# Kernel optimization log

Hardware: AMD Instinct MI355X
Metric: run time of the kernel (lower is better)

## Reference

```python
import jax, jax.numpy as jnp
import numpy as np

HEADS = 24
KV_HEADS = 6
HEAD_DIM = 64


def _partial_rope(x, cos, sin):
    # x: [B, H, S, head_dim]; cos/sin: [S, rot_dim]; rotate first rot_dim dims
    rot_dim = cos.shape[-1]
    x_rot, x_pass = x[..., :rot_dim], x[..., rot_dim:]
    half = rot_dim // 2
    # use_real_unbind_dim=-2: reshape (..., 2, half) then unbind -> first/second half
    x_real, x_imag = x_rot[..., :half], x_rot[..., half:]
    x_rotated = jnp.concatenate([-x_imag, x_real], axis=-1)
    out = x_rot * cos[None, None] + x_rotated * sin[None, None]
    return jnp.concatenate([out, x_pass], axis=-1)


def setup_inputs() -> dict:
    key = jax.random.key(0)
    ks = jax.random.split(key, 8)
    B, S, D = 2, 2048, 1536
    kv_dim = KV_HEADS * HEAD_DIM
    rot_dim = 32
    hidden_states = jax.random.normal(ks[0], (B, S, D), dtype=jnp.float32)
    # realistic rotary cos/sin from inv-freq angles
    pos = jnp.arange(S, dtype=jnp.float32)
    inv_freq = 1.0 / (10000.0 ** (jnp.arange(0, rot_dim, 2, dtype=jnp.float32) / rot_dim))
    ang = pos[:, None] * inv_freq[None, :]  # [S, rot_dim//2]
    ang = jnp.concatenate([ang, ang], axis=-1)  # [S, rot_dim]
    cos, sin = jnp.cos(ang), jnp.sin(ang)
    Wq = jax.random.normal(ks[1], (D, D), dtype=jnp.float32) * 0.02
    Wk = jax.random.normal(ks[2], (D, kv_dim), dtype=jnp.float32) * 0.02
    Wv = jax.random.normal(ks[3], (D, kv_dim), dtype=jnp.float32) * 0.02
    Wo = jax.random.normal(ks[4], (D, D), dtype=jnp.float32) * 0.02
    bo = jnp.zeros((D,), dtype=jnp.float32)
    return {"hidden_states": hidden_states, "cos": cos, "sin": sin,
            "Wq": Wq, "Wk": Wk, "Wv": Wv, "Wo": Wo, "bo": bo}


def reference(hidden_states, cos, sin, Wq, Wk, Wv, Wo, bo):
    B, S, D = hidden_states.shape
    residual = hidden_states
    q = hidden_states @ Wq  # [B,S,D]
    k = hidden_states @ Wk  # [B,S,kv_dim]
    v = hidden_states @ Wv
    q = q.reshape(B, S, HEADS, HEAD_DIM).transpose(0, 2, 1, 3)       # [B,H,S,d]
    k = k.reshape(B, S, KV_HEADS, HEAD_DIM).transpose(0, 2, 1, 3)    # [B,Hkv,S,d]
    v = v.reshape(B, S, KV_HEADS, HEAD_DIM).transpose(0, 2, 1, 3)
    rep = HEADS // KV_HEADS
    k = jnp.repeat(k, rep, axis=1)  # GQA repeat_interleave -> [B,H,S,d]
    v = jnp.repeat(v, rep, axis=1)
    # partial RoPE on query and key (self-attention)
    q = _partial_rope(q, cos, sin)
    k = _partial_rope(k, cos, sin)
    scale = 1.0 / jnp.sqrt(jnp.float32(HEAD_DIM))
    scores = jnp.einsum('bhqd,bhkd->bhqk', q, k) * scale
    probs = jax.nn.softmax(scores, axis=-1)
    out = jnp.einsum('bhqk,bhkd->bhqd', probs, v)
    out = out.transpose(0, 2, 1, 3).reshape(B, S, D)
    out = out @ Wo + bo
    return out + residual
```

## Files before the change

### kernel.cpp

```cpp
#include <hip/hip_runtime.h>

#define HEADS 24
#define KVH   6
#define HD    64
#define BB    2
#define SS    2048
#define DD    1536
#define KVD   384
#define QKD   1920
#define MM    4096

typedef unsigned short ushort_t;
typedef __attribute__((ext_vector_type(8))) short short8;
typedef __attribute__((ext_vector_type(4))) float f32x4;

__device__ __forceinline__ ushort_t f2bf(float f) {
    union { float f; unsigned u; } v; v.f = f;
    return (ushort_t)((v.u + 0x8000u) >> 16);
}
__device__ __forceinline__ ushort_t f2bf_trunc(float f) {
    union { float f; unsigned u; } v; v.f = f;
    return (ushort_t)(v.u >> 16);
}
__device__ __forceinline__ unsigned pk2(float a, float b) {
    union { float f; unsigned u; } x, y; x.f = a; y.f = b;
    return ((x.u + 0x8000u) >> 16) | (((y.u + 0x8000u) >> 16) << 16);
}
#if __has_builtin(__builtin_amdgcn_exp2f)
#define EXP2(x) __builtin_amdgcn_exp2f(x)
#else
#define EXP2(x) exp2f(x)
#endif
__device__ __forceinline__ void glds16(const void* g, void* l) {
    __builtin_amdgcn_global_load_lds(
        (const __attribute__((address_space(1))) void*)g,
        (__attribute__((address_space(3))) void*)l, 16, 0, 0);
}

__device__ __forceinline__ void tconv_body(const float* __restrict__ in,
                                           ushort_t* __restrict__ out,
                                           int R, int C, int cb, int rb)
{
    __shared__ ushort_t tile[32][33];
    const int tx = threadIdx.x & 31, ty = threadIdx.x >> 5;
    const int c0 = cb * 32, r0 = rb * 32;
#pragma unroll
    for (int i = 0; i < 4; ++i)
        tile[ty + i * 8][tx] = f2bf(in[(size_t)(r0 + ty + i * 8) * C + c0 + tx]);
    __syncthreads();
#pragma unroll
    for (int i = 0; i < 4; ++i)
        out[(size_t)(c0 + ty + i * 8) * R + r0 + tx] = tile[tx][ty + i * 8];
}

#define NCVT (MM * DD / 4 / 256)
__global__ __launch_bounds__(256) void k_prep(const float* __restrict__ HS,
                                              const float* __restrict__ Wq,
                                              const float* __restrict__ Wk,
                                              const float* __restrict__ Wv,
                                              const float* __restrict__ Wo,
                                              ushort_t* __restrict__ Xbf,
                                              ushort_t* __restrict__ Wqt,
                                              ushort_t* __restrict__ Wkt,
                                              ushort_t* __restrict__ Wvt,
                                              ushort_t* __restrict__ Wot)
{
    int bid = blockIdx.x;
    if (bid < NCVT) {
        int i = bid * 256 + threadIdx.x;
        float4 v = ((const float4*)HS)[i];
        uint2 o = { pk2(v.x, v.y), pk2(v.z, v.w) };
        ((uint2*)Xbf)[i] = o;
        return;
    }
    bid -= NCVT;
    if (bid < 2304) { tconv_body(Wq, Wqt, DD, DD,  bid % 48, bid / 48); return; }
    bid -= 2304;
    if (bid < 576)  { tconv_body(Wk, Wkt, DD, KVD, bid % 12, bid / 12); return; }
    bid -= 576;
    if (bid < 576)  { tconv_body(Wv, Wvt, DD, KVD, bid % 12, bid / 12); return; }
    bid -= 576;
    tconv_body(Wo, Wot, DD, DD, bid % 48, bid / 48);
}

__global__ __launch_bounds__(256) void k_qkv_mfma(const ushort_t* __restrict__ Xbf,
                                                  const ushort_t* __restrict__ Wqt,
                                                  const ushort_t* __restrict__ Wkt,
                                                  const float* __restrict__ cosb,
                                                  const float* __restrict__ sinb,
                                                  ushort_t* __restrict__ QKVb)
{
    __shared__ ushort_t As[128][32];
    __shared__ ushort_t Bs[128][32];
    const int t = threadIdx.x, lane = t & 63, wave = t >> 6;
    const int n16 = lane & 15, quad = lane >> 4;
    const int wr = wave >> 1, wc = wave & 1;
    const int nt = blockIdx.x;
    const int n0 = nt * 128;
    const int m0 = blockIdx.y * 128;
    const ushort_t* Bt; int nl, isq;
    if (nt < 12) { Bt = Wqt; nl = n0;      isq = 1; }
    else         { Bt = Wkt; nl = n0 - DD; isq = 0; }

    const int srow = lane >> 2;
    const int scol = (lane & 3) * 8;
    const size_t aoff0 = (size_t)(m0 + wave * 16 + srow) * DD + scol;
    const size_t aoff1 = (size_t)(m0 + (wave + 4) * 16 + srow) * DD + scol;
    const size_t boff0 = (size_t)(nl + wave * 16 + srow) * DD + scol;
    const size_t boff1 = (size_t)(nl + (wave + 4) * 16 + srow) * DD + scol;
    ushort_t* lA0 = &As[wave * 16][0];
    ushort_t* lA1 = &As[(wave + 4) * 16][0];
    ushort_t* lB0 = &Bs[wave * 16][0];
    ushort_t* lB1 = &Bs[(wave + 4) * 16][0];

    f32x4 acc[4][4] = {};
    for (int k0 = 0; k0 < DD; k0 += 32) {
        __syncthreads();
        glds16(Xbf + aoff0 + k0, lA0);
        glds16(Xbf + aoff1 + k0, lA1);
        glds16(Bt  + boff0 + k0, lB0);
        glds16(Bt  + boff1 + k0, lB1);
        __syncthreads();
        short8 af[4], bf8[4];
#pragma unroll
        for (int i = 0; i < 4; ++i) af[i]  = *(const short8*)&As[wr * 64 + i * 16 + n16][quad * 8];
#pragma unroll
        for (int j = 0; j < 4; ++j) bf8[j] = *(const short8*)&Bs[wc * 64 + j * 16 + n16][quad * 8];
#pragma unroll
        for (int i = 0; i < 4; ++i)
#pragma unroll
            for (int j = 0; j < 4; ++j)
                acc[i][j] = __builtin_amdgcn_mfma_f32_16x16x32_bf16(af[i], bf8[j], acc[i][j], 0, 0, 0);
    }

    const float QSC = 0.18033688011112042f;
#pragma unroll
    for (int i = 0; i < 4; ++i) {
#pragma unroll
        for (int r = 0; r < 4; ++r) {
            const int row = m0 + wr * 64 + i * 16 + quad * 4 + r;
            ushort_t* outp = QKVb + (size_t)row * QKD + n0 + wc * 64 + n16;
            float v0 = acc[i][0][r], v1 = acc[i][1][r];
            float v2 = acc[i][2][r], v3 = acc[i][3][r];
            {
                const int s = row & (SS - 1);
                float c0 = cosb[s * 32 + n16],      s0 = sinb[s * 32 + n16];
                float c1 = cosb[s * 32 + 16 + n16], s1 = sinb[s * 32 + 16 + n16];
                float nr = v0 * c0 - v1 * s0;
                float ni = v1 * c1 + v0 * s1;
                v0 = nr; v1 = ni;
            }
            if (isq) { v0 *= QSC; v1 *= QSC; v2 *= QSC; v3 *= QSC; }
            outp[0]  = f2bf(v0);
            outp[16] = f2bf(v1);
            outp[32] = f2bf(v2);
            outp[48] = f2bf(v3);
        }
    }
}

__global__ __launch_bounds__(256) void k_vtg(const ushort_t* __restrict__ Wvt,
                                             const ushort_t* __restrict__ Xbf,
                                             ushort_t* __restrict__ VT)
{
    __shared__ ushort_t As[64][32];
    __shared__ ushort_t Bs[128][32];
    const int t = threadIdx.x, lane = t & 63, wave = t >> 6;
    const int n16 = lane & 15, quad = lane >> 4;
    const int wr = wave >> 1, wc = wave & 1;
    const int n0 = blockIdx.x * 128;
    const int m0 = blockIdx.y * 64;

    const int srow = lane >> 2;
    const int scol = (lane & 3) * 8;
    const size_t aoff  = (size_t)(m0 + wave * 16 + srow) * DD + scol;
    const size_t boff0 = (size_t)(n0 + wave * 32 + srow) * DD + scol;
    const size_t boff1 = boff0 + (size_t)16 * DD;
    ushort_t* lA  = &As[wave * 16][0];
    ushort_t* lB0 = &Bs[wave * 32][0];
    ushort_t* lB1 = &Bs[wave * 32 + 16][0];

    f32x4 acc[2][4] = {};
    for (int k0 = 0; k0 < DD; k0 += 32) {
        __syncthreads();
        glds16(Wvt + aoff  + k0, lA);
        glds16(Xbf + boff0 + k0, lB0);
        glds16(Xbf + boff1 + k0, lB1);
        __syncthreads();
        short8 af[2], bf8[4];
#pragma unroll
        for (int i = 0; i < 2; ++i) af[i]  = *(const short8*)&As[wr * 32 + i * 16 + n16][quad * 8];
#pragma unroll
        for (int j = 0; j < 4; ++j) bf8[j] = *(const short8*)&Bs[wc * 64 + j * 16 + n16][quad * 8];
#pragma unroll
        for (int i = 0; i < 2; ++i)
#pragma unroll
            for (int j = 0; j < 4; ++j)
                acc[i][j] = __builtin_amdgcn_mfma_f32_16x16x32_bf16(af[i], bf8[j], acc[i][j], 0, 0, 0);
    }

    const int b = n0 >> 11;
#pragma unroll
    for (int i = 0; i < 2; ++i)
#pragma unroll
        for (int r = 0; r < 4; ++r) {
            const int c = m0 + wr * 32 + i * 16 + quad * 4 + r;
            ushort_t* op = VT + ((size_t)b * KVD + c) * SS + (n0 & (SS - 1)) + wc * 64 + n16;
#pragma unroll
            for (int j = 0; j < 4; ++j)
                op[j * 16] = f2bf(acc[i][j][r]);
        }
}

__global__ __launch_bounds__(256) void k_attn(const ushort_t* __restrict__ QKVb,
                                              const ushort_t* __restrict__ VT,
                                              ushort_t* __restrict__ AOb)
{
    __shared__ __align__(16) ushort_t Ks[64][72];
    __shared__ __align__(16) ushort_t Vs[64][72];
    __shared__ __align__(16) ushort_t Ps[128][76];

    const int t    = threadIdx.x;
    const int wave = t >> 6;
    const int quad = (t >> 4) & 3;
    const int n16  = t & 15;
    const int q0   = blockIdx.x * 128;
    const int h    = blockIdx.y;
    const int b    = blockIdx.z;
    const int kh   = h >> 2;

    const int sr = t >> 2;
    const int sc = (t & 3) * 8;
    const int vc = (t & 3) * 16;

    short8 qf[2][2];
#pragma unroll
    for (int m = 0; m < 2; ++m)
#pragma unroll
        for (int kc = 0; kc < 2; ++kc)
            qf[m][kc] = *(const short8*)(QKVb +
                (size_t)(b * SS + q0 + wave * 32 + m * 16 + n16) * QKD +
                h * HD + kc * 32 + quad * 8);

    float l_p[2][4] = {};
    f32x4 acc_o[2][4] = {};

    const ushort_t* Kbase = QKVb + (size_t)(b * SS) * QKD + DD + kh * HD;
    const ushort_t* Vbase = VT + ((size_t)b * KVD + kh * 64) * SS;

    for (int kt = 0; kt < SS / 64; ++kt) {
        const int k0 = kt * 64;
        __syncthreads();
        {
            const ushort_t* Kg = Kbase + (size_t)(k0 + sr) * QKD + sc;
            *(uint4*)&Ks[sr][sc]      = *(const uint4*)(Kg);
            *(uint4*)&Ks[sr][sc + 32] = *(const uint4*)(Kg + 32);
            const ushort_t* Vg = Vbase + (size_t)sr * SS + k0 + vc;
            *(uint4*)&Vs[sr][vc]      = *(const uint4*)(Vg);
            *(uint4*)&Vs[sr][vc + 8]  = *(const uint4*)(Vg + 8);
        }
        __syncthreads();

        f32x4 s_acc[2][4] = {};
#pragma unroll
        for (int kc = 0; kc < 2; ++kc) {
            short8 bf[4];
#pragma unroll
            for (int jj = 0; jj < 4; ++jj)
                bf[jj] = *(const short8*)&Ks[jj * 16 + n16][kc * 32 + quad * 8];
#pragma unroll
            for (int m = 0; m < 2; ++m)
#pragma unroll
                for (int jj = 0; jj < 4; ++jj)
                    s_acc[m][jj] = __builtin_amdgcn_mfma_f32_16x16x32_bf16(
                        qf[m][kc], bf[jj], s_acc[m][jj], 0, 0, 0);
        }

#pragma unroll
        for (int m = 0; m < 2; ++m)
#pragma unroll
            for (int r = 0; r < 4; ++r) {
                float p0 = EXP2(s_acc[m][0][r]);
                float p1 = EXP2(s_acc[m][1][r]);
                float p2 = EXP2(s_acc[m][2][r]);
                float p3 = EXP2(s_acc[m][3][r]);
                ushort_t* pr = &Ps[wave * 32 + m * 16 + quad * 4 + r][n16];
                pr[0]  = f2bf_trunc(p0);
                pr[16] = f2bf_trunc(p1);
                pr[32] = f2bf_trunc(p2);
                pr[48] = f2bf_trunc(p3);
                l_p[m][r] += (p0 + p1) + (p2 + p3);
            }

#pragma unroll
        for (int kc = 0; kc < 2; ++kc) {
            short8 vb[4];
#pragma unroll
            for (int dd = 0; dd < 4; ++dd)
                vb[dd] = *(const short8*)&Vs[dd * 16 + n16][kc * 32 + quad * 8];
#pragma unroll
            for (int m = 0; m < 2; ++m) {
                short8 pa = *(const short8*)&Ps[wave * 32 + m * 16 + n16][kc * 32 + quad * 8];
#pragma unroll
                for (int dd = 0; dd < 4; ++dd)
                    acc_o[m][dd] = __builtin_amdgcn_mfma_f32_16x16x32_bf16(
                        pa, vb[dd], acc_o[m][dd], 0, 0, 0);
            }
        }
    }

#pragma unroll
    for (int m = 0; m < 2; ++m) {
        float inv[4];
#pragma unroll
        for (int r = 0; r < 4; ++r) {
            float s = l_p[m][r];
#pragma unroll
            for (int msk = 1; msk < 16; msk <<= 1)
                s += __shfl_xor(s, msk);
            inv[r] = 1.0f / s;
        }
#pragma unroll
        for (int dd = 0; dd < 4; ++dd)
#pragma unroll
            for (int r = 0; r < 4; ++r) {
                int q = q0 + wave * 32 + m * 16 + quad * 4 + r;
                AOb[(size_t)(b * SS + q) * DD + h * HD + dd * 16 + n16] =
                    f2bf(acc_o[m][dd][r] * inv[r]);
            }
    }
}

__global__ __launch_bounds__(256) void k_out_mfma(const ushort_t* __restrict__ AOb,
                                                  const ushort_t* __restrict__ Wot,
                                                  const float* __restrict__ bo,
                                                  const float* __restrict__ HS,
                                                  float* __restrict__ out)
{
    __shared__ ushort_t As[64][32];
    __shared__ ushort_t Bs[128][32];
    const int t = threadIdx.x, lane = t & 63, wave = t >> 6;
    const int n16 = lane & 15, quad = lane >> 4;
    const int wr = wave >> 1, wc = wave & 1;
    const int n0 = blockIdx.x * 128;
    const int m0 = blockIdx.y * 64;

    const int srow = lane >> 2;
    const int scol = (lane & 3) * 8;
    const size_t aoff  = (size_t)(m0 + wave * 16 + srow) * DD + scol;
    const size_t boff0 = (size_t)(n0 + wave * 32 + srow) * DD + scol;
    const size_t boff1 = boff0 + (size_t)16 * DD;
    ushort_t* lA  = &As[wave * 16][0];
    ushort_t* lB0 = &Bs[wave * 32][0];
    ushort_t* lB1 = &Bs[wave * 32 + 16][0];

    f32x4 acc[2][4] = {};
    for (int k0 = 0; k0 < DD; k0 += 32) {
        __syncthreads();
        glds16(AOb + aoff  + k0, lA);
        glds16(Wot + boff0 + k0, lB0);
        glds16(Wot + boff1 + k0, lB1);
        __syncthreads();
        short8 af[2], bf8[4];
#pragma unroll
        for (int i = 0; i < 2; ++i) af[i]  = *(const short8*)&As[wr * 32 + i * 16 + n16][quad * 8];
#pragma unroll
        for (int j = 0; j < 4; ++j) bf8[j] = *(const short8*)&Bs[wc * 64 + j * 16 + n16][quad * 8];
#pragma unroll
        for (int i = 0; i < 2; ++i)
#pragma unroll
            for (int j = 0; j < 4; ++j)
                acc[i][j] = __builtin_amdgcn_mfma_f32_16x16x32_bf16(af[i], bf8[j], acc[i][j], 0, 0, 0);
    }

    const int colb = n0 + wc * 64 + n16;
    float bo4[4];
#pragma unroll
    for (int j = 0; j < 4; ++j) bo4[j] = bo[colb + j * 16];
#pragma unroll
    for (int i = 0; i < 2; ++i) {
#pragma unroll
        for (int r = 0; r < 4; ++r) {
            const int row = m0 + wr * 32 + i * 16 + quad * 4 + r;
            float* op = out + (size_t)row * DD + colb;
            const float* hp = HS + (size_t)row * DD + colb;
#pragma unroll
            for (int j = 0; j < 4; ++j)
                op[j * 16] = acc[i][j][r] + bo4[j] + hp[j * 16];
        }
    }
}

extern "C" void kernel_launch(void* const* d_in, const int* in_sizes, int n_in,
                              void* d_out, int out_size, void* d_ws, size_t ws_size,
                              hipStream_t stream)
{
    const float* HS   = (const float*)d_in[0];
    const float* cosb = (const float*)d_in[1];
    const float* sinb = (const float*)d_in[2];
    const float* Wq   = (const float*)d_in[3];
    const float* Wk   = (const float*)d_in[4];
    const float* Wv   = (const float*)d_in[5];
    const float* Wo   = (const float*)d_in[6];
    const float* bo   = (const float*)d_in[7];
    float* out = (float*)d_out;

    ushort_t* Xbf  = (ushort_t*)d_ws;
    ushort_t* QKVb = Xbf  + (size_t)MM * DD;
    ushort_t* AOb  = QKVb + (size_t)MM * QKD;
    ushort_t* Wqt  = AOb  + (size_t)MM * DD;
    ushort_t* Wkt  = Wqt  + (size_t)DD * DD;
    ushort_t* Wvt  = Wkt  + (size_t)KVD * DD;
    ushort_t* Wot  = Wvt  + (size_t)KVD * DD;
    ushort_t* VT   = Wot  + (size_t)DD * DD;

    const int nprep = NCVT + 2304 + 576 + 576 + 2304;
    k_prep    <<<dim3(nprep), 256, 0, stream>>>(HS, Wq, Wk, Wv, Wo,
                                                Xbf, Wqt, Wkt, Wvt, Wot);
    k_qkv_mfma<<<dim3(QKD / 128, MM / 128), 256, 0, stream>>>(Xbf, Wqt, Wkt, cosb, sinb, QKVb);
    k_vtg     <<<dim3(MM / 128, KVD / 64),  256, 0, stream>>>(Wvt, Xbf, VT);
    k_attn    <<<dim3(SS / 128, HEADS, BB), 256, 0, stream>>>(QKVb, VT, AOb);
    k_out_mfma<<<dim3(DD / 128, MM / 64),   256, 0, stream>>>(AOb, Wot, bo, HS, out);
}
```

Before: 288.2 us.

## Merge QKV and V-transpose GEMMs into one launch; pad attention LDS tiles

```diff
diff --git a/kernel.cpp b/kernel.cpp
--- a/kernel.cpp
+++ b/kernel.cpp
@@ -12,6 +12,7 @@
 
 typedef unsigned short ushort_t;
 typedef __attribute__((ext_vector_type(8))) short short8;
+typedef __attribute__((ext_vector_type(4))) short short4v;
 typedef __attribute__((ext_vector_type(4))) float f32x4;
 
 __device__ __forceinline__ ushort_t f2bf(float f) {
@@ -31,6 +32,11 @@
 #else
 #define EXP2(x) exp2f(x)
 #endif
+__device__ __forceinline__ short8 lds_frag8(const ushort_t* p) {
+    short4v lo = *(const short4v*)p;
+    short4v hi = *(const short4v*)(p + 4);
+    return __builtin_shufflevector(lo, hi, 0, 1, 2, 3, 4, 5, 6, 7);
+}
 __device__ __forceinline__ void glds16(const void* g, void* l) {
     __builtin_amdgcn_global_load_lds(
         (const __attribute__((address_space(1))) void*)g,
@@ -83,141 +89,135 @@
     tconv_body(Wo, Wot, DD, DD, bid % 48, bid / 48);
 }
 
-__global__ __launch_bounds__(256) void k_qkv_mfma(const ushort_t* __restrict__ Xbf,
-                                                  const ushort_t* __restrict__ Wqt,
-                                                  const ushort_t* __restrict__ Wkt,
-                                                  const float* __restrict__ cosb,
-                                                  const float* __restrict__ sinb,
-                                                  ushort_t* __restrict__ QKVb)
+__global__ __launch_bounds__(256) void k_proj(const ushort_t* __restrict__ Xbf,
+                                              const ushort_t* __restrict__ Wqt,
+                                              const ushort_t* __restrict__ Wkt,
+                                              const ushort_t* __restrict__ Wvt,
+                                              const float* __restrict__ cosb,
+                                              const float* __restrict__ sinb,
+                                              ushort_t* __restrict__ QKVb,
+                                              ushort_t* __restrict__ VT)
 {
     __shared__ ushort_t As[128][32];
     __shared__ ushort_t Bs[128][32];
     const int t = threadIdx.x, lane = t & 63, wave = t >> 6;
     const int n16 = lane & 15, quad = lane >> 4;
     const int wr = wave >> 1, wc = wave & 1;
-    const int nt = blockIdx.x;
-    const int n0 = nt * 128;
-    const int m0 = blockIdx.y * 128;
-    const ushort_t* Bt; int nl, isq;
-    if (nt < 12) { Bt = Wqt; nl = n0;      isq = 1; }
-    else         { Bt = Wkt; nl = n0 - DD; isq = 0; }
-
     const int srow = lane >> 2;
     const int scol = (lane & 3) * 8;
-    const size_t aoff0 = (size_t)(m0 + wave * 16 + srow) * DD + scol;
-    const size_t aoff1 = (size_t)(m0 + (wave + 4) * 16 + srow) * DD + scol;
-    const size_t boff0 = (size_t)(nl + wave * 16 + srow) * DD + scol;
-    const size_t boff1 = (size_t)(nl + (wave + 4) * 16 + srow) * DD + scol;
-    ushort_t* lA0 = &As[wave * 16][0];
-    ushort_t* lA1 = &As[(wave + 4) * 16][0];
-    ushort_t* lB0 = &Bs[wave * 16][0];
-    ushort_t* lB1 = &Bs[(wave + 4) * 16][0];
-
-    f32x4 acc[4][4] = {};
-    for (int k0 = 0; k0 < DD; k0 += 32) {
-        __syncthreads();
-        glds16(Xbf + aoff0 + k0, lA0);
-        glds16(Xbf + aoff1 + k0, lA1);
-        glds16(Bt  + boff0 + k0, lB0);
-        glds16(Bt  + boff1 + k0, lB1);
-        __syncthreads();
-        short8 af[4], bf8[4];
-#pragma unroll
-        for (int i = 0; i < 4; ++i) af[i]  = *(const short8*)&As[wr * 64 + i * 16 + n16][quad * 8];
-#pragma unroll
-        for (int j = 0; j < 4; ++j) bf8[j] = *(const short8*)&Bs[wc * 64 + j * 16 + n16][quad * 8];
-#pragma unroll
-        for (int i = 0; i < 4; ++i)
-#pragma unroll
-            for (int j = 0; j < 4; ++j)
-                acc[i][j] = __builtin_amdgcn_mfma_f32_16x16x32_bf16(af[i], bf8[j], acc[i][j], 0, 0, 0);
-    }
-
-    const float QSC = 0.18033688011112042f;
-#pragma unroll
-    for (int i = 0; i < 4; ++i) {
-#pragma unroll
-        for (int r = 0; r < 4; ++r) {
-            const int row = m0 + wr * 64 + i * 16 + quad * 4 + r;
-            ushort_t* outp = QKVb + (size_t)row * QKD + n0 + wc * 64 + n16;
-            float v0 = acc[i][0][r], v1 = acc[i][1][r];
-            float v2 = acc[i][2][r], v3 = acc[i][3][r];
-            {
-                const int s = row & (SS - 1);
-                float c0 = cosb[s * 32 + n16],      s0 = sinb[s * 32 + n16];
-                float c1 = cosb[s * 32 + 16 + n16], s1 = sinb[s * 32 + 16 + n16];
-                float nr = v0 * c0 - v1 * s0;
-                float ni = v1 * c1 + v0 * s1;
-                v0 = nr; v1 = ni;
+
+    if (blockIdx.x < 480) {
+        const int nt = blockIdx.x % 15;
+        const int n0 = nt * 128;
+        const int m0 = (blockIdx.x / 15) * 128;
+        const ushort_t* Bt; int nl, isq;
+        if (nt < 12) { Bt = Wqt; nl = n0;      isq = 1; }
+        else         { Bt = Wkt; nl = n0 - DD; isq = 0; }
+
+        const size_t aoff0 = (size_t)(m0 + wave * 16 + srow) * DD + scol;
+        const size_t aoff1 = (size_t)(m0 + (wave + 4) * 16 + srow) * DD + scol;
+        const size_t boff0 = (size_t)(nl + wave * 16 + srow) * DD + scol;
+        const size_t boff1 = (size_t)(nl + (wave + 4) * 16 + srow) * DD + scol;
+        ushort_t* lA0 = &As[wave * 16][0];
+        ushort_t* lA1 = &As[(wave + 4) * 16][0];
+        ushort_t* lB0 = &Bs[wave * 16][0];
+        ushort_t* lB1 = &Bs[(wave + 4) * 16][0];
+
+        f32x4 acc[4][4] = {};
+        for (int k0 = 0; k0 < DD; k0 += 32) {
+            __syncthreads();
+            glds16(Xbf + aoff0 + k0, lA0);
+            glds16(Xbf + aoff1 + k0, lA1);
+            glds16(Bt  + boff0 + k0, lB0);
+            glds16(Bt  + boff1 + k0, lB1);
+            __syncthreads();
+            short8 af[4], bf8[4];
+#pragma unroll
+            for (int i = 0; i < 4; ++i) af[i]  = *(const short8*)&As[wr * 64 + i * 16 + n16][quad * 8];
+#pragma unroll
+            for (int j = 0; j < 4; ++j) bf8[j] = *(const short8*)&Bs[wc * 64 + j * 16 + n16][quad * 8];
+#pragma unroll
+            for (int i = 0; i < 4; ++i)
+#pragma unroll
+                for (int j = 0; j < 4; ++j)
+                    acc[i][j] = __builtin_amdgcn_mfma_f32_16x16x32_bf16(af[i], bf8[j], acc[i][j], 0, 0, 0);
+        }
+
+        const float QSC = 0.18033688011112042f;
+#pragma unroll
+        for (int i = 0; i < 4; ++i) {
+#pragma unroll
+            for (int r = 0; r < 4; ++r) {
+                const int row = m0 + wr * 64 + i * 16 + quad * 4 + r;
+                ushort_t* outp = QKVb + (size_t)row * QKD + n0 + wc * 64 + n16;
+                float v0 = acc[i][0][r], v1 = acc[i][1][r];
+                float v2 = acc[i][2][r], v3 = acc[i][3][r];
+                {
+                    const int s = row & (SS - 1);
+                    float c0 = cosb[s * 32 + n16],      s0 = sinb[s * 32 + n16];
+                    float c1 = cosb[s * 32 + 16 + n16], s1 = sinb[s * 32 + 16 + n16];
+                    float nr = v0 * c0 - v1 * s0;
+                    float ni = v1 * c1 + v0 * s1;
+                    v0 = nr; v1 = ni;
+                }
+                if (isq) { v0 *= QSC; v1 *= QSC; v2 *= QSC; v3 *= QSC; }
+                outp[0]  = f2bf(v0);
+                outp[16] = f2bf(v1);
+                outp[32] = f2bf(v2);
+                outp[48] = f2bf(v3);
             }
-            if (isq) { v0 *= QSC; v1 *= QSC; v2 *= QSC; v3 *= QSC; }
-            outp[0]  = f2bf(v0);
-            outp[16] = f2bf(v1);
-            outp[32] = f2bf(v2);
-            outp[48] = f2bf(v3);
-        }
-    }
-}
-
-__global__ __launch_bounds__(256) void k_vtg(const ushort_t* __restrict__ Wvt,
-                                             const ushort_t* __restrict__ Xbf,
-                                             ushort_t* __restrict__ VT)
-{
-    __shared__ ushort_t As[64][32];
-    __shared__ ushort_t Bs[128][32];
-    const int t = threadIdx.x, lane = t & 63, wave = t >> 6;
-    const int n16 = lane & 15, quad = lane >> 4;
-    const int wr = wave >> 1, wc = wave & 1;
-    const int n0 = blockIdx.x * 128;
-    const int m0 = blockIdx.y * 64;
-
-    const int srow = lane >> 2;
-    const int scol = (lane & 3) * 8;
-    const size_t aoff  = (size_t)(m0 + wave * 16 + srow) * DD + scol;
-    const size_t boff0 = (size_t)(n0 + wave * 32 + srow) * DD + scol;
-    const size_t boff1 = boff0 + (size_t)16 * DD;
-    ushort_t* lA  = &As[wave * 16][0];
-    ushort_t* lB0 = &Bs[wave * 32][0];
-    ushort_t* lB1 = &Bs[wave * 32 + 16][0];
-
-    f32x4 acc[2][4] = {};
-    for (int k0 = 0; k0 < DD; k0 += 32) {
-        __syncthreads();
-        glds16(Wvt + aoff  + k0, lA);
-        glds16(Xbf + boff0 + k0, lB0);
-        glds16(Xbf + boff1 + k0, lB1);
-        __syncthreads();
-        short8 af[2], bf8[4];
-#pragma unroll
-        for (int i = 0; i < 2; ++i) af[i]  = *(const short8*)&As[wr * 32 + i * 16 + n16][quad * 8];
-#pragma unroll
-        for (int j = 0; j < 4; ++j) bf8[j] = *(const short8*)&Bs[wc * 64 + j * 16 + n16][quad * 8];
+        }
+    } else {
+        const int vb = blockIdx.x - 480;
+        const int n0 = (vb & 31) * 128;
+        const int m0 = (vb >> 5) * 64;
+
+        const size_t aoff  = (size_t)(m0 + wave * 16 + srow) * DD + scol;
+        const size_t boff0 = (size_t)(n0 + wave * 32 + srow) * DD + scol;
+        const size_t boff1 = boff0 + (size_t)16 * DD;
+        ushort_t* lA  = &As[wave * 16][0];
+        ushort_t* lB0 = &Bs[wave * 32][0];
+        ushort_t* lB1 = &Bs[wave * 32 + 16][0];
+
+        f32x4 acc[2][4] = {};
+        for (int k0 = 0; k0 < DD; k0 += 32) {
+            __syncthreads();
+            glds16(Wvt + aoff  + k0, lA);
+            glds16(Xbf + boff0 + k0, lB0);
+            glds16(Xbf + boff1 + k0, lB1);
+            __syncthreads();
+            short8 af[2], bf8[4];
+#pragma unroll
+            for (int i = 0; i < 2; ++i) af[i]  = *(const short8*)&As[wr * 32 + i * 16 + n16][quad * 8];
+#pragma unroll
+            for (int j = 0; j < 4; ++j) bf8[j] = *(const short8*)&Bs[wc * 64 + j * 16 + n16][quad * 8];
+#pragma unroll
+            for (int i = 0; i < 2; ++i)
+#pragma unroll
+                for (int j = 0; j < 4; ++j)
+                    acc[i][j] = __builtin_amdgcn_mfma_f32_16x16x32_bf16(af[i], bf8[j], acc[i][j], 0, 0, 0);
+        }
+
+        const int b = n0 >> 11;
 #pragma unroll
         for (int i = 0; i < 2; ++i)
 #pragma unroll
-            for (int j = 0; j < 4; ++j)
-                acc[i][j] = __builtin_amdgcn_mfma_f32_16x16x32_bf16(af[i], bf8[j], acc[i][j], 0, 0, 0);
-    }
-
-    const int b = n0 >> 11;
-#pragma unroll
-    for (int i = 0; i < 2; ++i)
-#pragma unroll
-        for (int r = 0; r < 4; ++r) {
-            const int c = m0 + wr * 32 + i * 16 + quad * 4 + r;
-            ushort_t* op = VT + ((size_t)b * KVD + c) * SS + (n0 & (SS - 1)) + wc * 64 + n16;
-#pragma unroll
-            for (int j = 0; j < 4; ++j)
-                op[j * 16] = f2bf(acc[i][j][r]);
-        }
+            for (int r = 0; r < 4; ++r) {
+                const int c = m0 + wr * 32 + i * 16 + quad * 4 + r;
+                ushort_t* op = VT + ((size_t)b * KVD + c) * SS + (n0 & (SS - 1)) + wc * 64 + n16;
+#pragma unroll
+                for (int j = 0; j < 4; ++j)
+                    op[j * 16] = f2bf(acc[i][j][r]);
+            }
+    }
 }
 
 __global__ __launch_bounds__(256) void k_attn(const ushort_t* __restrict__ QKVb,
                                               const ushort_t* __restrict__ VT,
                                               ushort_t* __restrict__ AOb)
 {
-    __shared__ __align__(16) ushort_t Ks[64][72];
-    __shared__ __align__(16) ushort_t Vs[64][72];
+    __shared__ __align__(16) ushort_t Ks[64][76];
+    __shared__ __align__(16) ushort_t Vs[64][76];
     __shared__ __align__(16) ushort_t Ps[128][76];
 
     const int t    = threadIdx.x;
@@ -253,11 +253,19 @@
         __syncthreads();
         {
             const ushort_t* Kg = Kbase + (size_t)(k0 + sr) * QKD + sc;
-            *(uint4*)&Ks[sr][sc]      = *(const uint4*)(Kg);
-            *(uint4*)&Ks[sr][sc + 32] = *(const uint4*)(Kg + 32);
+            uint4 kv0 = *(const uint4*)(Kg);
+            uint4 kv1 = *(const uint4*)(Kg + 32);
+            *(uint2*)&Ks[sr][sc]          = make_uint2(kv0.x, kv0.y);
+            *(uint2*)&Ks[sr][sc + 4]      = make_uint2(kv0.z, kv0.w);
+            *(uint2*)&Ks[sr][sc + 32]     = make_uint2(kv1.x, kv1.y);
+            *(uint2*)&Ks[sr][sc + 36]     = make_uint2(kv1.z, kv1.w);
             const ushort_t* Vg = Vbase + (size_t)sr * SS + k0 + vc;
-            *(uint4*)&Vs[sr][vc]      = *(const uint4*)(Vg);
-            *(uint4*)&Vs[sr][vc + 8]  = *(const uint4*)(Vg + 8);
+            uint4 vv0 = *(const uint4*)(Vg);
+            uint4 vv1 = *(const uint4*)(Vg + 8);
+            *(uint2*)&Vs[sr][vc]          = make_uint2(vv0.x, vv0.y);
+            *(uint2*)&Vs[sr][vc + 4]      = make_uint2(vv0.z, vv0.w);
+            *(uint2*)&Vs[sr][vc + 8]      = make_uint2(vv1.x, vv1.y);
+            *(uint2*)&Vs[sr][vc + 12]     = make_uint2(vv1.z, vv1.w);
         }
         __syncthreads();
 
@@ -267,7 +275,7 @@
             short8 bf[4];
 #pragma unroll
             for (int jj = 0; jj < 4; ++jj)
-                bf[jj] = *(const short8*)&Ks[jj * 16 + n16][kc * 32 + quad * 8];
+                bf[jj] = lds_frag8(&Ks[jj * 16 + n16][kc * 32 + quad * 8]);
 #pragma unroll
             for (int m = 0; m < 2; ++m)
 #pragma unroll
@@ -297,10 +305,10 @@
             short8 vb[4];
 #pragma unroll
             for (int dd = 0; dd < 4; ++dd)
-                vb[dd] = *(const short8*)&Vs[dd * 16 + n16][kc * 32 + quad * 8];
+                vb[dd] = lds_frag8(&Vs[dd * 16 + n16][kc * 32 + quad * 8]);
 #pragma unroll
             for (int m = 0; m < 2; ++m) {
-                short8 pa = *(const short8*)&Ps[wave * 32 + m * 16 + n16][kc * 32 + quad * 8];
+                short8 pa = lds_frag8(&Ps[wave * 32 + m * 16 + n16][kc * 32 + quad * 8]);
 #pragma unroll
                 for (int dd = 0; dd < 4; ++dd)
                     acc_o[m][dd] = __builtin_amdgcn_mfma_f32_16x16x32_bf16(
@@ -417,8 +425,8 @@
     const int nprep = NCVT + 2304 + 576 + 576 + 2304;
     k_prep    <<<dim3(nprep), 256, 0, stream>>>(HS, Wq, Wk, Wv, Wo,
                                                 Xbf, Wqt, Wkt, Wvt, Wot);
-    k_qkv_mfma<<<dim3(QKD / 128, MM / 128), 256, 0, stream>>>(Xbf, Wqt, Wkt, cosb, sinb, QKVb);
-    k_vtg     <<<dim3(MM / 128, KVD / 64),  256, 0, stream>>>(Wvt, Xbf, VT);
+    k_proj    <<<dim3(480 + 192), 256, 0, stream>>>(Xbf, Wqt, Wkt, Wvt,
+                                                    cosb, sinb, QKVb, VT);
     k_attn    <<<dim3(SS / 128, HEADS, BB), 256, 0, stream>>>(QKVb, VT, AOb);
     k_out_mfma<<<dim3(DD / 128, MM / 64),   256, 0, stream>>>(AOb, Wot, bo, HS, out);
 }
```

Result: faster. 270.3 us (-6.2%).
